# Kernel tuning notes

Hardware: AMD Instinct MI355X
Metric: run time of the kernel (lower is better)

The kernel has to match this reference:

```python
import jax, jax.numpy as jnp
import numpy as np

TEMPERATURE = 22.627417  # ~sqrt(512)


def setup_inputs() -> dict:
    key = jax.random.key(0)
    ks = jax.random.split(key, 7)
    B, NP, NQ, D = 4, 256, 256, 512
    return {
        "q": jax.random.normal(ks[0], (B, NP, D), jnp.float32),
        "k": jax.random.normal(ks[1], (B, NP, D), jnp.float32),
        "v": jax.random.normal(ks[2], (B, NP, D), jnp.float32),
        "query": jax.random.normal(ks[3], (B, NQ, D), jnp.float32),
        "query_q": jax.random.normal(ks[4], (B, NQ, D), jnp.float32),
        "query_k": jax.random.normal(ks[5], (B, NP, D), jnp.float32),
        "query_v": jax.random.normal(ks[6], (B, NQ, D), jnp.float32),
    }


def reference(q, k, v, query, query_q, query_k, query_v):
    # Self-attention block over prototypes: [B, NP, NP]
    scores = jnp.einsum("bpd,bqd->bpq", q, k) / TEMPERATURE
    log_attn = jax.nn.log_softmax(scores, axis=2)
    attn = jax.nn.softmax(scores, axis=2)
    # NOTE: torch.bmm(attn, v) in the original is dead code (overwritten), so it is skipped.

    # Query-gated attention: [B, NQ, NP]
    q_scores = jnp.einsum("bnd,bpd->bnp", query_q, query_k) / TEMPERATURE
    query_attn = jax.nn.softmax(q_scores, axis=2)

    # Gated broadcast combine: [B, NQ, NP, D]
    # query_attn * v_rep + query_attn * query_v == query_attn * (v + query_v)
    gate = query_attn[:, :, :, None]            # [B, NQ, NP, 1]
    combined = v[:, None, :, :] + query_v[:, :, None, :]  # [B, NQ, NP, D]
    output = gate * combined
    return (output, attn, log_attn)
```

## Files before the change

kernel.cpp:

```cpp
#include <hip/hip_runtime.h>
#include <math.h>

#define BB   4
#define NP   256
#define NQ   256
#define DD   512
#define DD4  (DD / 4)

typedef float f32x4 __attribute__((ext_vector_type(4)));

static constexpr float kScale = 1.0f / 22.627417f;

__global__ __launch_bounds__(256) void gate_kernel(
    const float* __restrict__ qq,
    const float* __restrict__ qk,
    float* __restrict__ outf)
{
    const int b  = blockIdx.y;
    const int n0 = blockIdx.x * 4;
    const int t  = threadIdx.x;

    const f32x4* krow = (const f32x4*)(qk + ((size_t)b * NP + t) * DD);
    const float* qb   = qq + ((size_t)b * NQ + n0) * DD;

    float acc[4] = {0.f, 0.f, 0.f, 0.f};
    #pragma unroll 8
    for (int d4 = 0; d4 < DD4; ++d4) {
        const f32x4 kv = krow[d4];
        #pragma unroll
        for (int r = 0; r < 4; ++r) {
            const float* qr = qb + r * DD + d4 * 4;
            acc[r] += qr[0] * kv.x + qr[1] * kv.y + qr[2] * kv.z + qr[3] * kv.w;
        }
    }

    __shared__ __align__(16) float ss[4][256];
    #pragma unroll
    for (int r = 0; r < 4; ++r) ss[r][t] = acc[r] * kScale;
    __syncthreads();

    const int r = t >> 6;
    const int g = t & 63;
    const f32x4 sv = ((const f32x4*)ss[r])[g];

    float m = fmaxf(fmaxf(sv.x, sv.y), fmaxf(sv.z, sv.w));
    #pragma unroll
    for (int off = 32; off >= 1; off >>= 1) m = fmaxf(m, __shfl_xor(m, off, 64));

    f32x4 ev;
    ev.x = expf(sv.x - m); ev.y = expf(sv.y - m);
    ev.z = expf(sv.z - m); ev.w = expf(sv.w - m);
    float s = (ev.x + ev.y) + (ev.z + ev.w);
    #pragma unroll
    for (int off = 32; off >= 1; off >>= 1) s += __shfl_xor(s, off, 64);
    const float inv = 1.0f / s;

    const int n  = n0 + r;
    const int ng = n >> 3, nr = n & 7;
    const int c0 = 4 * g;
    const int pr = c0 >> 5;
    float* slot = outf
        + (((size_t)(b * NQ + (ng << 3))) * NP + (pr << 5)) * DD
        + nr * 32 + (c0 & 31);
    *(f32x4*)slot = ev * inv;
}

__global__ __launch_bounds__(256) void store_kernel(
    const float* __restrict__ q,
    const float* __restrict__ k,
    const f32x4* __restrict__ v4,
    const f32x4* __restrict__ qv4,
    float* __restrict__ outf,
    float* __restrict__ attn_out,
    float* __restrict__ logattn_out)
{
    __shared__ __align__(16) float smem[4 * 256];
    const int t = threadIdx.x;

    if (blockIdx.x < 1024u) {
        const int idx  = blockIdx.x;
        const int b    = idx >> 8;
        const int rest = idx & 255;
        const int n0   = (rest >> 3) << 3;
        const int p0   = (rest & 7) << 5;

        const float* slot = outf + (((size_t)(b * NQ + n0)) * NP + p0) * DD;
        smem[t] = slot[t];
        __syncthreads();

        const int d4 = t & (DD4 - 1);
        const int po = t >> 7;
        const f32x4* qvb = qv4 + ((size_t)(b * NQ + n0)) * DD4 + d4;
        f32x4 qvr[8];
        #pragma unroll
        for (int r = 0; r < 8; ++r) qvr[r] = qvb[(size_t)r * DD4];

        const f32x4* vcol  = v4 + ((size_t)b * NP) * DD4 + d4;
        f32x4*       obase = (f32x4*)outf + (((size_t)(b * NQ + n0)) * NP) * DD4 + d4;

        #pragma unroll 2
        for (int pi = 0; pi < 16; ++pi) {
            const int p  = p0 + 2 * pi + po;
            const int pc = 2 * pi + po;
            const f32x4 vv = vcol[(size_t)p * DD4];
            #pragma unroll
            for (int r = 0; r < 8; ++r) {
                const float gpn = smem[r * 32 + pc];
                __builtin_nontemporal_store((vv + qvr[r]) * gpn,
                    obase + ((size_t)r * NP + p) * DD4);
            }
        }
    } else {
        const int idx = blockIdx.x - 1024;
        const int b   = idx >> 6;
        const int p0  = (idx & 63) * 4;

        const f32x4* krow = (const f32x4*)(k + ((size_t)b * NP + t) * DD);
        const float* qb   = q + ((size_t)b * NP + p0) * DD;

        float acc[4] = {0.f, 0.f, 0.f, 0.f};
        #pragma unroll 8
        for (int d4 = 0; d4 < DD4; ++d4) {
            const f32x4 kv = krow[d4];
            #pragma unroll
            for (int r = 0; r < 4; ++r) {
                const float* qr = qb + r * DD + d4 * 4;
                acc[r] += qr[0] * kv.x + qr[1] * kv.y + qr[2] * kv.z + qr[3] * kv.w;
            }
        }

        float (*ss)[256] = (float (*)[256])smem;
        #pragma unroll
        for (int r = 0; r < 4; ++r) ss[r][t] = acc[r] * kScale;
        __syncthreads();

        const int r = t >> 6;
        const int g = t & 63;
        const f32x4 sv = ((const f32x4*)ss[r])[g];

        float m = fmaxf(fmaxf(sv.x, sv.y), fmaxf(sv.z, sv.w));
        #pragma unroll
        for (int off = 32; off >= 1; off >>= 1)
            m = fmaxf(m, __shfl_xor(m, off, 64));

        f32x4 ev;
        ev.x = expf(sv.x - m); ev.y = expf(sv.y - m);
        ev.z = expf(sv.z - m); ev.w = expf(sv.w - m);
        float s = (ev.x + ev.y) + (ev.z + ev.w);
        #pragma unroll
        for (int off = 32; off >= 1; off >>= 1) s += __shfl_xor(s, off, 64);

        const float inv = 1.0f / s;
        const float lse = logf(s);

        const size_t base = ((size_t)b * NP + (p0 + r)) * 256;
        ((f32x4*)(attn_out + base))[g] = ev * inv;
        f32x4 lg;
        lg.x = (sv.x - m) - lse; lg.y = (sv.y - m) - lse;
        lg.z = (sv.z - m) - lse; lg.w = (sv.w - m) - lse;
        ((f32x4*)(logattn_out + base))[g] = lg;
    }
}

extern "C" void kernel_launch(void* const* d_in, const int* in_sizes, int n_in,
                              void* d_out, int out_size, void* d_ws, size_t ws_size,
                              hipStream_t stream) {
    const float* q  = (const float*)d_in[0];
    const float* k  = (const float*)d_in[1];
    const float* v  = (const float*)d_in[2];
    const float* qq = (const float*)d_in[4];
    const float* qk = (const float*)d_in[5];
    const float* qv = (const float*)d_in[6];

    float* out = (float*)d_out;
    const size_t out_elems = (size_t)BB * NQ * NP * DD;
    float* attn_out    = out + out_elems;
    float* logattn_out = attn_out + (size_t)BB * NP * 256;

    gate_kernel<<<dim3(NQ / 4, BB), 256, 0, stream>>>(qq, qk, out);

    store_kernel<<<1280, 256, 0, stream>>>(
        q, k, (const f32x4*)v, (const f32x4*)qv, out, attn_out, logattn_out);
}
```

Measured before the change: 145.9 us.

## Move gate matrix to workspace and use grid-stride chunked store loop

The gate softmax is now written to a separate workspace buffer instead of being stashed inside the output tensor, so the store kernel no longer needs the shared-memory staging step or its barrier. The store path becomes a persistent grid-stride loop over 131072 contiguous 4KB chunks across 1792 blocks. Each chunk loads its scalar gate value and the v and query_v rows and writes the output with contiguous nontemporal stores. This trades register reuse of query_v rows across 8 n values for simpler, fully contiguous writes, at the cost of more v/qv reads, which should mostly hit cache.

Result: faster. 134.7 us (-7.6%).

```diff
diff --git a/kernel.cpp b/kernel.cpp
--- a/kernel.cpp
+++ b/kernel.cpp
@@ -7,6 +7,9 @@
 #define DD   512
 #define DD4  (DD / 4)
 
+#define NSTORE       1792
+#define TOTAL_CHUNKS 131072
+
 typedef float f32x4 __attribute__((ext_vector_type(4)));
 
 static constexpr float kScale = 1.0f / 22.627417f;
@@ -14,7 +17,7 @@
 __global__ __launch_bounds__(256) void gate_kernel(
     const float* __restrict__ qq,
     const float* __restrict__ qk,
-    float* __restrict__ outf)
+    float* __restrict__ gws)
 {
     const int b  = blockIdx.y;
     const int n0 = blockIdx.x * 4;
@@ -53,16 +56,8 @@
     float s = (ev.x + ev.y) + (ev.z + ev.w);
     #pragma unroll
     for (int off = 32; off >= 1; off >>= 1) s += __shfl_xor(s, off, 64);
-    const float inv = 1.0f / s;
 
-    const int n  = n0 + r;
-    const int ng = n >> 3, nr = n & 7;
-    const int c0 = 4 * g;
-    const int pr = c0 >> 5;
-    float* slot = outf
-        + (((size_t)(b * NQ + (ng << 3))) * NP + (pr << 5)) * DD
-        + nr * 32 + (c0 & 31);
-    *(f32x4*)slot = ev * inv;
+    ((f32x4*)(gws + ((size_t)b * NQ + n0 + r) * NP))[g] = ev * (1.0f / s);
 }
 
 __global__ __launch_bounds__(256) void store_kernel(
@@ -70,48 +65,33 @@
     const float* __restrict__ k,
     const f32x4* __restrict__ v4,
     const f32x4* __restrict__ qv4,
-    float* __restrict__ outf,
+    const float* __restrict__ gws,
+    f32x4* __restrict__ out4,
     float* __restrict__ attn_out,
     float* __restrict__ logattn_out)
 {
-    __shared__ __align__(16) float smem[4 * 256];
     const int t = threadIdx.x;
 
-    if (blockIdx.x < 1024u) {
-        const int idx  = blockIdx.x;
-        const int b    = idx >> 8;
-        const int rest = idx & 255;
-        const int n0   = (rest >> 3) << 3;
-        const int p0   = (rest & 7) << 5;
+    if (blockIdx.x < (unsigned)NSTORE) {
+        const int h  = t >> 7;
+        const int d4 = t & (DD4 - 1);
 
-        const float* slot = outf + (((size_t)(b * NQ + n0)) * NP + p0) * DD;
-        smem[t] = slot[t];
-        __syncthreads();
+        for (int c = blockIdx.x; c < TOTAL_CHUNKS; c += NSTORE) {
+            const int b = c >> 15;
+            const int n = (c >> 7) & 255;
+            const int p = (2 * c + h) & 255;
 
-        const int d4 = t & (DD4 - 1);
-        const int po = t >> 7;
-        const f32x4* qvb = qv4 + ((size_t)(b * NQ + n0)) * DD4 + d4;
-        f32x4 qvr[8];
-        #pragma unroll
-        for (int r = 0; r < 8; ++r) qvr[r] = qvb[(size_t)r * DD4];
+            int gidx = (((b << 8) + n) << 8) + p;
+            gidx = __builtin_amdgcn_readfirstlane(gidx);
+            const float gpn = gws[gidx];
 
-        const f32x4* vcol  = v4 + ((size_t)b * NP) * DD4 + d4;
-        f32x4*       obase = (f32x4*)outf + (((size_t)(b * NQ + n0)) * NP) * DD4 + d4;
-
-        #pragma unroll 2
-        for (int pi = 0; pi < 16; ++pi) {
-            const int p  = p0 + 2 * pi + po;
-            const int pc = 2 * pi + po;
-            const f32x4 vv = vcol[(size_t)p * DD4];
-            #pragma unroll
-            for (int r = 0; r < 8; ++r) {
-                const float gpn = smem[r * 32 + pc];
-                __builtin_nontemporal_store((vv + qvr[r]) * gpn,
-                    obase + ((size_t)r * NP + p) * DD4);
-            }
+            const f32x4 vv  = v4[(((size_t)(b << 8) + p) << 7) + d4];
+            const f32x4 qvv = qv4[(((size_t)(b << 8) + n) << 7) + d4];
+            __builtin_nontemporal_store((vv + qvv) * gpn,
+                                        out4 + ((size_t)c << 8) + t);
         }
     } else {
-        const int idx = blockIdx.x - 1024;
+        const int idx = blockIdx.x - NSTORE;
         const int b   = idx >> 6;
         const int p0  = (idx & 63) * 4;
 
@@ -129,7 +109,7 @@
             }
         }
 
-        float (*ss)[256] = (float (*)[256])smem;
+        __shared__ __align__(16) float ss[4][256];
         #pragma unroll
         for (int r = 0; r < 4; ++r) ss[r][t] = acc[r] * kScale;
         __syncthreads();
@@ -177,8 +157,11 @@
     float* attn_out    = out + out_elems;
     float* logattn_out = attn_out + (size_t)BB * NP * 256;
 
-    gate_kernel<<<dim3(NQ / 4, BB), 256, 0, stream>>>(qq, qk, out);
+    float* gws = (float*)d_ws;
 
-    store_kernel<<<1280, 256, 0, stream>>>(
-        q, k, (const f32x4*)v, (const f32x4*)qv, out, attn_out, logattn_out);
+    gate_kernel<<<dim3(NQ / 4, BB), 256, 0, stream>>>(qq, qk, gws);
+
+    store_kernel<<<NSTORE + 256, 256, 0, stream>>>(
+        q, k, (const f32x4*)v, (const f32x4*)qv, gws,
+        (f32x4*)out, attn_out, logattn_out);
 }
```
